# Performance work log

Hardware: AMD Instinct MI355X
Metric: run time of the kernel (lower is better)

The kernel has to match this reference:

```python
import jax, jax.numpy as jnp
import numpy as np

K = 3      # kernel_size
P = 1      # padding (stride=1, dilation=1 so L_out == L)
C_IN = 512
C_OUT = 512


def setup_inputs() -> dict:
    key = jax.random.key(0)
    k1, k2, k3, k4 = jax.random.split(key, 4)
    x = jax.random.normal(k1, (8, C_IN, 4096), dtype=jnp.float32)
    # small offset weights so predicted sampling offsets stay near the base grid
    w_off = jax.random.normal(k2, (2 * K, C_IN, K), dtype=jnp.float32) * 0.01
    b_off = jnp.zeros((2 * K,), dtype=jnp.float32)
    w_conv = jax.random.normal(k3, (C_OUT, C_IN * K, 1), dtype=jnp.float32) * (1.0 / np.sqrt(C_IN * K))
    b_conv = jax.random.normal(k4, (C_OUT,), dtype=jnp.float32) * 0.01
    return {"x": x, "w_off": w_off, "b_off": b_off, "w_conv": w_conv, "b_conv": b_conv}


def reference(x, w_off, b_off, w_conv, b_conv):
    N, C, L = x.shape
    # offset prediction: Conv1d(C -> 2K, kernel=K, pad=P)
    offsets = jax.lax.conv_general_dilated(
        x, w_off, window_strides=(1,), padding=[(P, P)],
        dimension_numbers=("NCH", "OIH", "NCH")) + b_off[None, :, None]
    L_out = offsets.shape[2]
    # [N, 2K, L_out] -> [N, K, 2, L_out] -> [N, L_out, K, 2]; only [...,0] is used
    off = offsets.reshape(N, K, 2, L_out).transpose(0, 3, 1, 2)

    x_pad = jnp.pad(x, ((0, 0), (0, 0), (P, P)))  # [N, C, Lp]
    Lp = x_pad.shape[2]
    base = jnp.arange(Lp, dtype=x.dtype)[P:Lp - P]          # length L_out
    grid = jnp.clip(base[None, :, None] + off[..., 0], 0.0, Lp - 1)  # [N, L_out, K]
    left = jnp.floor(grid)
    right = jnp.minimum(left + 1.0, Lp - 1)
    alpha = grid - left                                       # [N, L_out, K]

    li = left.astype(jnp.int32).reshape(N, -1)
    ri = right.astype(jnp.int32).reshape(N, -1)
    gather = jax.vmap(lambda xp, i: xp[:, i])                 # per-sample gather along L
    x_left = gather(x_pad, li).reshape(N, C, L_out, K)
    x_right = gather(x_pad, ri).reshape(N, C, L_out, K)

    a = alpha.reshape(N, 1, L_out, K)
    x_deform = (1.0 - a) * x_left + a * x_right               # [N, C, L_out, K]
    # faithful to torch: permute(0,3,2,1) then raw view to [N, C*K, L_out]
    x_deform = x_deform.transpose(0, 3, 2, 1).reshape(N, C * K, L_out)
    # 1x1 conv == GEMM over channel dim
    return jnp.einsum("oi,nil->nol", w_conv[:, :, 0], x_deform) + b_conv[None, :, None]
```

## Files before the change

### kernel.cpp

```cpp
#include <hip/hip_runtime.h>
#include <stdint.h>

#define C_INN 512
#define C_OUTT 512
#define LL 4096
#define KDIM 1536

typedef __attribute__((ext_vector_type(8))) short bf16x8;
typedef __attribute__((ext_vector_type(4))) float f32x4;

static __device__ __forceinline__ uint16_t f2bf(float f) {
    union { float f; uint32_t u; } c; c.f = f;
    uint32_t u = c.u;
    uint32_t r = u + 0x7FFFu + ((u >> 16) & 1u);
    return (uint16_t)(r >> 16);
}

static __device__ __forceinline__ void gload_lds16(const uint16_t* g, uint16_t* l) {
    __builtin_amdgcn_global_load_lds(
        (const __attribute__((address_space(1))) uint32_t*)g,
        (__attribute__((address_space(3))) uint32_t*)l, 16, 0, 0);
}

__global__ void k_convA(const float* __restrict__ w, uint16_t* __restrict__ Ab) {
    int i = (blockIdx.x * 256 + threadIdx.x) * 4;
    float4 v = *(const float4*)(w + i);
    ushort4 o;
    o.x = f2bf(v.x); o.y = f2bf(v.y); o.z = f2bf(v.z); o.w = f2bf(v.w);
    *(ushort4*)(Ab + i) = o;
}

__global__ __launch_bounds__(256) void k_off1(const float* __restrict__ x,
        const float* __restrict__ wo, float* __restrict__ part) {
    const int split = blockIdx.x;
    const int tile  = blockIdx.y;
    const int n     = blockIdx.z;
    const int tid = threadIdx.x;
    const int w = tid >> 6, lane = tid & 63;
    const int lo0 = tile * 256;
    const int ch0 = split * 64;

    __shared__ float4 wq[64][3];
    for (int i = tid; i < 576; i += 256) {
        int cl = i / 9, r = i - cl * 9;
        int k = r / 3, t = r - k * 3;
        ((float*)wq)[cl * 12 + r] = wo[(2 * k) * 1536 + (ch0 + cl) * 3 + t];
    }
    __syncthreads();

    float4 a0 = {0,0,0,0}, a1 = {0,0,0,0}, a2 = {0,0,0,0};
    const float* xn = x + ((size_t)n * C_INN + ch0 + w * 16) * LL + lo0;
    #pragma unroll 4
    for (int it = 0; it < 16; ++it) {
        const float* xp = xn + (size_t)it * LL;
        float4 v = *(const float4*)(xp + 4 * lane);
        float xl = xp[(lo0 > 0) ? -1 : 0];
        float xr = xp[(lo0 < 3840) ? 256 : 255];
        float lm = __shfl_up(v.w, 1, 64);
        lm = (lane == 0) ? ((lo0 > 0) ? xl : 0.f) : lm;
        float rp = __shfl_down(v.x, 1, 64);
        rp = (lane == 63) ? ((lo0 < 3840) ? xr : 0.f) : rp;
        int cl = w * 16 + it;
        float4 q0 = wq[cl][0], q1 = wq[cl][1], q2 = wq[cl][2];
        a0.x += q0.x * lm   + q0.y * v.x + q0.z * v.y;
        a0.y += q0.x * v.x  + q0.y * v.y + q0.z * v.z;
        a0.z += q0.x * v.y  + q0.y * v.z + q0.z * v.w;
        a0.w += q0.x * v.z  + q0.y * v.w + q0.z * rp;
        a1.x += q0.w * lm   + q1.x * v.x + q1.y * v.y;
        a1.y += q0.w * v.x  + q1.x * v.y + q1.y * v.z;
        a1.z += q0.w * v.y  + q1.x * v.z + q1.y * v.w;
        a1.w += q0.w * v.z  + q1.x * v.w + q1.y * rp;
        a2.x += q1.z * lm   + q1.w * v.x + q2.x * v.y;
        a2.y += q1.z * v.x  + q1.w * v.y + q2.x * v.z;
        a2.z += q1.z * v.y  + q1.w * v.z + q2.x * v.w;
        a2.w += q1.z * v.z  + q1.w * v.w + q2.x * rp;
    }

    __shared__ float4 red[4][3][64];
    red[w][0][lane] = a0; red[w][1][lane] = a1; red[w][2][lane] = a2;
    __syncthreads();
    if (tid < 192) {
        int k = tid >> 6, l = tid & 63;
        float4 r0 = red[0][k][l], r1 = red[1][k][l], r2 = red[2][k][l], r3 = red[3][k][l];
        float4 s;
        s.x = r0.x + r1.x + r2.x + r3.x;
        s.y = r0.y + r1.y + r2.y + r3.y;
        s.z = r0.z + r1.z + r2.z + r3.z;
        s.w = r0.w + r1.w + r2.w + r3.w;
        float4* p4 = (float4*)part;
        p4[(size_t)(((n * 16 + tile) * 8 + split)) * 192 + k * 64 + l] = s;
    }
}

__global__ __launch_bounds__(256) void k_off2(const float* __restrict__ part,
        const float* __restrict__ bo, float2* __restrict__ liA) {
    const int b = blockIdx.x;
    const int n = b >> 4, tile = b & 15;
    const int tid = threadIdx.x;
    const int lo = tile * 256 + tid;
    #pragma unroll
    for (int k = 0; k < 3; ++k) {
        float s = 0.f;
        #pragma unroll
        for (int sp = 0; sp < 8; ++sp)
            s += part[(size_t)(b * 8 + sp) * 768 + k * 256 + tid];
        s += bo[2 * k];
        float g = fminf(fmaxf((float)(lo + 1) + s, 0.f), 4097.f);
        float lif = floorf(g);
        liA[((n * 3 + k) * 8 + (lo & 7)) * 512 + (lo >> 3)] = make_float2(lif, g - lif);
    }
}

__global__ __launch_bounds__(512) void k_build(const float* __restrict__ x,
        const float2* __restrict__ liA, uint16_t* __restrict__ Bt, int n0) {
    const int c0 = blockIdx.x * 4;
    const int nl = blockIdx.y;
    const int n  = n0 + nl;
    const int tid = threadIdx.x;
    __shared__ float xs[4][4232];
    #pragma unroll
    for (int c4 = 0; c4 < 4; ++c4) {
        const float* xr = x + ((size_t)n * C_INN + c0 + c4) * LL + tid * 8;
        float4 v0 = *(const float4*)xr;
        float4 v1 = *(const float4*)(xr + 4);
        int p = tid * 8;
        int sb = p + (p >> 5);
        float* xsp = xs[c4];
        xsp[sb + 0] = v0.x; xsp[sb + 1] = v0.y; xsp[sb + 2] = v0.z; xsp[sb + 3] = v0.w;
        xsp[sb + 4] = v1.x; xsp[sb + 5] = v1.y; xsp[sb + 6] = v1.z; xsp[sb + 7] = v1.w;
        if (tid == 0) xsp[4228] = 0.f;
    }
    __syncthreads();
    const int q = tid >> 6, lane = tid & 63;
    uint32_t* outp0 = (uint32_t*)(Bt + (size_t)(nl * LL + q * 512 + c0) * KDIM);
    #pragma unroll
    for (int k = 0; k < 3; ++k) {
        const float2* lp = liA + ((size_t)((n * 3 + k) * 8 + q)) * 512;
        #pragma unroll
        for (int jc = 0; jc < 4; ++jc) {
            float4 la = *(const float4*)(lp + jc * 128 + 2 * lane);
            int li0 = (int)la.x; float a0 = la.y;
            int li1 = (int)la.z; float a1 = la.w;
            int l0m = li0 - 1, l1m = li1 - 1;
            int iL0 = ((unsigned)l0m < 4096u) ? (l0m + (l0m >> 5)) : 4228;
            int iR0 = ((unsigned)li0 < 4096u) ? (li0 + (li0 >> 5)) : 4228;
            int iL1 = ((unsigned)l1m < 4096u) ? (l1m + (l1m >> 5)) : 4228;
            int iR1 = ((unsigned)li1 < 4096u) ? (li1 + (li1 >> 5)) : 4228;
            #pragma unroll
            for (int c4 = 0; c4 < 4; ++c4) {
                const float* xsp = xs[c4];
                float xl0 = xsp[iL0], xr0 = xsp[iR0];
                float xl1 = xsp[iL1], xr1 = xsp[iR1];
                float v0 = xl0 + a0 * (xr0 - xl0);
                float v1 = xl1 + a1 * (xr1 - xl1);
                uint32_t pk;
                asm("v_cvt_pk_bf16_f32 %0, %1, %2" : "=v"(pk) : "v"(v0), "v"(v1));
                outp0[(size_t)c4 * KDIM / 2 + k * 256 + jc * 64 + lane] = pk;
            }
        }
    }
}

#define SBAR() do { asm volatile("" ::: "memory"); __builtin_amdgcn_s_barrier(); asm volatile("" ::: "memory"); } while (0)
#define VMC(n) asm volatile("s_waitcnt vmcnt(" #n ")" ::: "memory")

__global__ __launch_bounds__(512, 2) void k_gemm(const uint16_t* __restrict__ Ab,
        const uint16_t* __restrict__ Bt, const float* __restrict__ bias,
        float* __restrict__ out, int n0) {
    const int bid = blockIdx.x;
    const int cpx = gridDim.x >> 3;
    const int swz = (bid & 7) * cpx + (bid >> 3);
    const int mt = swz & 1;
    const int nt = swz >> 1;
    const int row0 = mt * 256;
    const int col0 = nt * 256;
    const int tid = threadIdx.x;
    const int wv = tid >> 6, lane = tid & 63;
    const int wr = wv >> 2, wc = wv & 3;
    const int r16 = lane & 15, kg = lane >> 4;

    __shared__ uint16_t As[2][16384];
    __shared__ uint16_t Bs[2][16384];

    f32x4 acc[8][4] = {};

    float4 bpre[8];
    #pragma unroll
    for (int m = 0; m < 8; ++m)
        bpre[m] = *(const float4*)(bias + row0 + wr * 128 + m * 16 + kg * 4);

    const int sr  = tid >> 3;
    const int skc = (tid & 7) ^ (sr & 7);
    const uint16_t* Asrc = Ab + (size_t)(row0 + sr) * KDIM + skc * 8;
    const uint16_t* Bsrc = Bt + (size_t)(col0 + sr) * KDIM + skc * 8;

    const int xorw = (r16 & 7) * 8;
    const int kko0 = (kg * 8) ^ xorw;
    const int kko1 = (32 + kg * 8) ^ xorw;

    auto stageA = [&](int slot, int half, int kt) {
        const uint16_t* g = Asrc + (size_t)half * 128 * KDIM + kt * 64;
        uint16_t* l = &As[slot][half * 8192 + tid * 8];
        gload_lds16(g, l);
        gload_lds16(g + (size_t)64 * KDIM, l + 4096);
    };
    auto stageB = [&](int slot, int half, int kt) {
        const uint16_t* g = Bsrc + (size_t)half * 128 * KDIM + kt * 64;
        uint16_t* l = &Bs[slot][half * 8192 + tid * 8];
        gload_lds16(g, l);
        gload_lds16(g + (size_t)64 * KDIM, l + 4096);
    };

    bf16x8 af[2][2], bfr[4][2];

#define LDAQ(s, q) do { \
    af[0][0] = *(const bf16x8*)(&As[s][(wr*128 + (q)*32      + r16) * 64 + kko0]); \
    af[0][1] = *(const bf16x8*)(&As[s][(wr*128 + (q)*32      + r16) * 64 + kko1]); \
    af[1][0] = *(const bf16x8*)(&As[s][(wr*128 + (q)*32 + 16 + r16) * 64 + kko0]); \
    af[1][1] = *(const bf16x8*)(&As[s][(wr*128 + (q)*32 + 16 + r16) * 64 + kko1]); \
} while (0)

#define LDBALL(s) do { \
    _Pragma("unroll") \
    for (int nn = 0; nn < 4; ++nn) { \
        bfr[nn][0] = *(const bf16x8*)(&Bs[s][(wc*64 + nn*16 + r16) * 64 + kko0]); \
        bfr[nn][1] = *(const bf16x8*)(&Bs[s][(wc*64 + nn*16 + r16) * 64 + kko1]); \
    } \
} while (0)

#define MQ(q) do { \
    __builtin_amdgcn_s_setprio(1); \
    _Pragma("unroll") \
    for (int mi = 0; mi < 2; ++mi) { \
        _Pragma("unroll") \
        for (int nn = 0; nn < 4; ++nn) { \
            acc[(q)*2+mi][nn] = __builtin_amdgcn_mfma_f32_16x16x32_bf16(af[mi][0], bfr[nn][0], acc[(q)*2+mi][nn], 0, 0, 0); \
            acc[(q)*2+mi][nn] = __builtin_amdgcn_mfma_f32_16x16x32_bf16(af[mi][1], bfr[nn][1], acc[(q)*2+mi][nn], 0, 0, 0); \
        } \
    } \
    __builtin_amdgcn_s_setprio(0); \
} while (0)

    stageA(0, 0, 0); stageA(0, 1, 0);
    stageB(0, 0, 0); stageB(0, 1, 0);
    stageB(1, 0, 1); stageB(1, 1, 1);
    VMC(0);
    SBAR();

    for (int j = 0; j < 11; ++j) {
        const int kt1  = 2 * j + 1;
        const int ktn0 = 2 * j + 2;
        const int ktn1 = 2 * j + 3;
        LDBALL(0); LDAQ(0, 0); stageA(1, 0, kt1);
        SBAR(); MQ(0);
        LDAQ(0, 1); stageA(1, 1, kt1);
        SBAR(); MQ(1);
        LDAQ(0, 2); stageB(0, 0, ktn0);
        SBAR(); MQ(2);
        LDAQ(0, 3); stageB(0, 1, ktn0);
        SBAR(); MQ(3); VMC(4); SBAR();
        LDBALL(1); LDAQ(1, 0); stageA(0, 0, ktn0);
        SBAR(); MQ(0);
        LDAQ(1, 1); stageA(0, 1, ktn0);
        SBAR(); MQ(1);
        LDAQ(1, 2); stageB(1, 0, ktn1);
        SBAR(); MQ(2);
        LDAQ(1, 3); stageB(1, 1, ktn1);
        SBAR(); MQ(3); VMC(4); SBAR();
    }

    LDBALL(0); LDAQ(0, 0); stageA(1, 0, 23);
    SBAR(); MQ(0);
    LDAQ(0, 1); stageA(1, 1, 23);
    SBAR(); MQ(1);
    LDAQ(0, 2);
    SBAR(); MQ(2);
    LDAQ(0, 3);
    SBAR(); MQ(3); VMC(0); SBAR();
    LDBALL(1); LDAQ(1, 0);
    SBAR(); MQ(0);
    LDAQ(1, 1);
    SBAR(); MQ(1);
    LDAQ(1, 2);
    SBAR(); MQ(2);
    LDAQ(1, 3);
    SBAR(); MQ(3);

    const int rb = col0 + wc * 64;
    #pragma unroll
    for (int m = 0; m < 8; ++m) {
        #pragma unroll
        for (int e = 0; e < 4; ++e) {
            int o = row0 + wr * 128 + m * 16 + kg * 4 + e;
            float bv = ((const float*)&bpre[m])[e];
            #pragma unroll
            for (int nn = 0; nn < 4; ++nn) {
                int rc = rb + nn * 16 + r16;
                int nli = rc >> 12;
                int lpos = rc & 4095;
                out[((size_t)(n0 + nli) * C_OUTT + o) * LL + lpos] = acc[m][nn][e] + bv;
            }
        }
    }
#undef LDAQ
#undef LDBALL
#undef MQ
}

extern "C" void kernel_launch(void* const* d_in, const int* in_sizes, int n_in,
                              void* d_out, int out_size, void* d_ws, size_t ws_size,
                              hipStream_t stream) {
    const float* x  = (const float*)d_in[0];
    const float* wo = (const float*)d_in[1];
    const float* bo = (const float*)d_in[2];
    const float* wc = (const float*)d_in[3];
    const float* bc = (const float*)d_in[4];
    float* out = (float*)d_out;

    char* ws = (char*)d_ws;
    uint16_t* Ab   = (uint16_t*)ws;
    float2*   liA  = (float2*)(ws + 1572864);
    float*    part = (float*)(ws + 2359296);
    uint16_t* Bt   = (uint16_t*)(ws + 5505024);
    const size_t fixed = 5505024;
    int nc = 8;
    while (nc > 1 && fixed + (size_t)nc * 12582912ull > ws_size) nc >>= 1;

    k_convA<<<768, 256, 0, stream>>>(wc, Ab);
    k_off1<<<dim3(8, 16, 8), 256, 0, stream>>>(x, wo, part);
    k_off2<<<128, 256, 0, stream>>>(part, bo, liA);
    for (int n0 = 0; n0 < 8; n0 += nc) {
        k_build<<<dim3(128, nc), 512, 0, stream>>>(x, liA, Bt, n0);
        k_gemm<<<2 * nc * 16, 512, 0, stream>>>(Ab, Bt, bc, out, n0);
    }
}
```

Baseline: 107.5 us.

## Double GEMM block to 1024 threads with half the rows per wave

The GEMM kernel now launches 1024 threads per block instead of 512, laid out as a 4x4 wave grid. Each wave owns a 64-row by 64-column slice, so the accumulators drop from 8x4 to 4x4 fragments. Each thread issues one global-to-LDS load per stage instead of two, and the vmcnt waits are adjusted to match. Bias is now read at the epilogue instead of preloaded. The goal is more waves to hide latency and lower per-thread register use. The risks are the aggressive launch bound (1024, 4), which may force register limits and spills, and extra barrier overhead across twice as many waves.

New measurement: 112.2 us. +4.3%, slower.

```diff
diff --git a/kernel.cpp b/kernel.cpp
--- a/kernel.cpp
+++ b/kernel.cpp
@@ -164,7 +164,7 @@
 #define SBAR() do { asm volatile("" ::: "memory"); __builtin_amdgcn_s_barrier(); asm volatile("" ::: "memory"); } while (0)
 #define VMC(n) asm volatile("s_waitcnt vmcnt(" #n ")" ::: "memory")
 
-__global__ __launch_bounds__(512, 2) void k_gemm(const uint16_t* __restrict__ Ab,
+__global__ __launch_bounds__(1024, 4) void k_gemm(const uint16_t* __restrict__ Ab,
         const uint16_t* __restrict__ Bt, const float* __restrict__ bias,
         float* __restrict__ out, int n0) {
     const int bid = blockIdx.x;
@@ -182,12 +182,7 @@
     __shared__ uint16_t As[2][16384];
     __shared__ uint16_t Bs[2][16384];
 
-    f32x4 acc[8][4] = {};
-
-    float4 bpre[8];
-    #pragma unroll
-    for (int m = 0; m < 8; ++m)
-        bpre[m] = *(const float4*)(bias + row0 + wr * 128 + m * 16 + kg * 4);
+    f32x4 acc[4][4] = {};
 
     const int sr  = tid >> 3;
     const int skc = (tid & 7) ^ (sr & 7);
@@ -199,25 +194,19 @@
     const int kko1 = (32 + kg * 8) ^ xorw;
 
     auto stageA = [&](int slot, int half, int kt) {
-        const uint16_t* g = Asrc + (size_t)half * 128 * KDIM + kt * 64;
-        uint16_t* l = &As[slot][half * 8192 + tid * 8];
-        gload_lds16(g, l);
-        gload_lds16(g + (size_t)64 * KDIM, l + 4096);
+        gload_lds16(Asrc + (size_t)half * 128 * KDIM + kt * 64,
+                    &As[slot][half * 8192 + tid * 8]);
     };
     auto stageB = [&](int slot, int half, int kt) {
-        const uint16_t* g = Bsrc + (size_t)half * 128 * KDIM + kt * 64;
-        uint16_t* l = &Bs[slot][half * 8192 + tid * 8];
-        gload_lds16(g, l);
-        gload_lds16(g + (size_t)64 * KDIM, l + 4096);
+        gload_lds16(Bsrc + (size_t)half * 128 * KDIM + kt * 64,
+                    &Bs[slot][half * 8192 + tid * 8]);
     };
 
-    bf16x8 af[2][2], bfr[4][2];
-
-#define LDAQ(s, q) do { \
-    af[0][0] = *(const bf16x8*)(&As[s][(wr*128 + (q)*32      + r16) * 64 + kko0]); \
-    af[0][1] = *(const bf16x8*)(&As[s][(wr*128 + (q)*32      + r16) * 64 + kko1]); \
-    af[1][0] = *(const bf16x8*)(&As[s][(wr*128 + (q)*32 + 16 + r16) * 64 + kko0]); \
-    af[1][1] = *(const bf16x8*)(&As[s][(wr*128 + (q)*32 + 16 + r16) * 64 + kko1]); \
+    bf16x8 af[2], bfr[4][2];
+
+#define LDAQ(s, m) do { \
+    af[0] = *(const bf16x8*)(&As[s][(wr*64 + (m)*16 + r16) * 64 + kko0]); \
+    af[1] = *(const bf16x8*)(&As[s][(wr*64 + (m)*16 + r16) * 64 + kko1]); \
 } while (0)
 
 #define LDBALL(s) do { \
@@ -228,15 +217,12 @@
     } \
 } while (0)
 
-#define MQ(q) do { \
+#define MQ(m) do { \
     __builtin_amdgcn_s_setprio(1); \
     _Pragma("unroll") \
-    for (int mi = 0; mi < 2; ++mi) { \
-        _Pragma("unroll") \
-        for (int nn = 0; nn < 4; ++nn) { \
-            acc[(q)*2+mi][nn] = __builtin_amdgcn_mfma_f32_16x16x32_bf16(af[mi][0], bfr[nn][0], acc[(q)*2+mi][nn], 0, 0, 0); \
-            acc[(q)*2+mi][nn] = __builtin_amdgcn_mfma_f32_16x16x32_bf16(af[mi][1], bfr[nn][1], acc[(q)*2+mi][nn], 0, 0, 0); \
-        } \
+    for (int nn = 0; nn < 4; ++nn) { \
+        acc[m][nn] = __builtin_amdgcn_mfma_f32_16x16x32_bf16(af[0], bfr[nn][0], acc[m][nn], 0, 0, 0); \
+        acc[m][nn] = __builtin_amdgcn_mfma_f32_16x16x32_bf16(af[1], bfr[nn][1], acc[m][nn], 0, 0, 0); \
     } \
     __builtin_amdgcn_s_setprio(0); \
 } while (0)
@@ -258,7 +244,7 @@
         LDAQ(0, 2); stageB(0, 0, ktn0);
         SBAR(); MQ(2);
         LDAQ(0, 3); stageB(0, 1, ktn0);
-        SBAR(); MQ(3); VMC(4); SBAR();
+        SBAR(); MQ(3); VMC(2); SBAR();
         LDBALL(1); LDAQ(1, 0); stageA(0, 0, ktn0);
         SBAR(); MQ(0);
         LDAQ(1, 1); stageA(0, 1, ktn0);
@@ -266,7 +252,7 @@
         LDAQ(1, 2); stageB(1, 0, ktn1);
         SBAR(); MQ(2);
         LDAQ(1, 3); stageB(1, 1, ktn1);
-        SBAR(); MQ(3); VMC(4); SBAR();
+        SBAR(); MQ(3); VMC(2); SBAR();
     }
 
     LDBALL(0); LDAQ(0, 0); stageA(1, 0, 23);
@@ -288,11 +274,11 @@
 
     const int rb = col0 + wc * 64;
     #pragma unroll
-    for (int m = 0; m < 8; ++m) {
+    for (int m = 0; m < 4; ++m) {
         #pragma unroll
         for (int e = 0; e < 4; ++e) {
-            int o = row0 + wr * 128 + m * 16 + kg * 4 + e;
-            float bv = ((const float*)&bpre[m])[e];
+            int o = row0 + wr * 64 + m * 16 + kg * 4 + e;
+            float bv = bias[o];
             #pragma unroll
             for (int nn = 0; nn < 4; ++nn) {
                 int rc = rb + nn * 16 + r16;
@@ -331,6 +317,6 @@
     k_off2<<<128, 256, 0, stream>>>(part, bo, liA);
     for (int n0 = 0; n0 < 8; n0 += nc) {
         k_build<<<dim3(128, nc), 512, 0, stream>>>(x, liA, Bt, n0);
-        k_gemm<<<2 * nc * 16, 512, 0, stream>>>(Ab, Bt, bc, out, n0);
-    }
-}
+        k_gemm<<<2 * nc * 16, 1024, 0, stream>>>(Ab, Bt, bc, out, n0);
+    }
+}
```
